# Performance work log

Hardware: AMD Instinct MI355X
Metric: run time of the kernel (lower is better)

## Reference

```python
import jax, jax.numpy as jnp
import numpy as np

R = 2
TAU = 0.1
EPS = 1e-7

# normalized 3x3 Sobel kernels (kornia SpatialGradient, normalized=True -> /8)
_GX = jnp.array([[-1., 0., 1.], [-2., 0., 2.], [-1., 0., 1.]], dtype=jnp.float32) / 8.0
_GY = _GX.T

K = 2 * R - 1  # 3
_HORIZ = jnp.zeros((K, K), jnp.float32).at[R - 1, :].set(1.0)
_VERT = jnp.zeros((K, K), jnp.float32).at[:, R - 1].set(1.0)
_LEAD = jnp.eye(K, dtype=jnp.float32)
_CNT = jnp.fliplr(jnp.eye(K, dtype=jnp.float32))


def _conv2d_same(x, k2d, mode):
    # depthwise 'same' cross-correlation, x: (B,C,H,W), k2d: (k,k)
    C = x.shape[1]
    p = k2d.shape[-1] // 2
    xp = jnp.pad(x, ((0, 0), (0, 0), (p, p), (p, p)), mode=mode)
    kern = jnp.broadcast_to(k2d[None, None], (C, 1) + k2d.shape)
    return jax.lax.conv_general_dilated(
        xp, kern, (1, 1), 'VALID',
        dimension_numbers=('NCHW', 'OIHW', 'NCHW'),
        feature_group_count=C)


def _grad_angles(t):
    # kornia SpatialGradient pads with replicate ('edge')
    gx = _conv2d_same(t, _GX, 'edge')
    gy = _conv2d_same(t, _GY, 'edge')
    grad_xx = _conv2d_same(gx, _GX, 'edge')
    grad_xy = _conv2d_same(gy, _GX, 'edge')
    grad_yy = _conv2d_same(gy, _GY, 'edge')
    theta = jnp.arctan(grad_yy * jnp.sign(-grad_xy + EPS) / (grad_xx + EPS))
    angle = theta * (180.0 / np.pi)
    return jnp.where(angle < 0, angle + 180.0, angle)


def _nms_loss(true_labels, pred_labels):
    angle = _grad_angles(true_labels)
    mask = (true_labels > 0).astype(jnp.float32)

    th_h = mask * (((angle >= 0) & (angle < 22.5)) | ((angle >= 157.5) & (angle < 180))).astype(jnp.float32)
    th_cd = mask * ((angle >= 22.5) & (angle < 67.5)).astype(jnp.float32)
    th_v = mask * ((angle >= 67.5) & (angle < 112.5)).astype(jnp.float32)
    th_ld = mask * ((angle > 112.5) & (angle < 157.5)).astype(jnp.float32)

    e = jnp.exp(pred_labels * TAU)

    def term(th, kern):
        f = _conv2d_same(e, kern, 'reflect')  # kornia filter2D default border 'reflect'
        return th * jnp.log(jnp.clip(e / (f + EPS), EPS, 1.0))

    total = (term(th_h, _HORIZ) + term(th_v, _VERT) +
             term(th_ld, _LEAD) + term(th_cd, _CNT))
    # sum over (C,H,W) per sample, mean over batch, negate
    return -jnp.mean(jnp.sum(total, axis=(1, 2, 3)))


def setup_inputs() -> dict:
    key = jax.random.key(0)
    k1, k2 = jax.random.split(key)
    B, C, H, W = 4, 19, 512, 512
    true_labels = jax.random.normal(k1, (B, C, H, W), dtype=jnp.float32)
    pred_labels = jax.random.normal(k2, (B, C, H, W), dtype=jnp.float32)
    return {"true_labels": true_labels, "pred_labels": pred_labels}


def reference(true_labels, pred_labels):
    return _nms_loss(true_labels, pred_labels)
```

## Files before the change

### kernel.cpp

```cpp
#include <hip/hip_runtime.h>

#define BAND 16
#define NITER (BAND + 4)
#define NSLOT 1024

__global__ __launch_bounds__(256) void nms_loss_kernel(
    const float* __restrict__ tl, const float* __restrict__ pl,
    double* __restrict__ acc_d, float* __restrict__ acc_f,
    int H, int W)
{
    const int y0  = blockIdx.x * BAND;
    const int ch  = blockIdx.y;
    const float* tc = tl + (size_t)ch * H * W;
    const float* pc = pl + (size_t)ch * H * W;
    const int tid  = threadIdx.x;
    const int lane = tid & 63;
    const int c0 = tid << 1;
    const int oa = min(max(c0 - 2, 0), W - 2);
    const int oc = min(c0 + 2, W - 2);
    const bool xedge = (c0 == 0) || (c0 == W - 2);

    float P1h[5][2], P2h[5][2], P3h[5][2];
    float eh[3][4], tch[3][2];
    float tA[6], pA[6], tB[6], pB[6];

    #define LOADROW(I, T6, P6) {                                                   \
        int tr_ = y0 - 2 + (I); tr_ = min(max(tr_, 0), H - 1);                      \
        int pr_ = y0 - 3 + (I); pr_ = pr_ < 0 ? -pr_ : (pr_ >= H ? 2*H-2-pr_ : pr_);\
        const float* tb_ = tc + (size_t)tr_ * W;                                    \
        const float* pb_ = pc + (size_t)pr_ * W;                                    \
        float2 a_ = *(const float2*)(tb_ + oa), b_ = *(const float2*)(tb_ + c0),    \
               c_ = *(const float2*)(tb_ + oc);                                     \
        T6[0]=a_.x; T6[1]=a_.y; T6[2]=b_.x; T6[3]=b_.y; T6[4]=c_.x; T6[5]=c_.y;     \
        a_ = *(const float2*)(pb_ + oa); b_ = *(const float2*)(pb_ + c0);           \
        c_ = *(const float2*)(pb_ + oc);                                            \
        P6[0]=a_.x; P6[1]=a_.y; P6[2]=b_.x; P6[3]=b_.y; P6[4]=c_.x; P6[5]=c_.y; }

    #define CONSUME(T6, P6, SP, SE) {                                               \
        const int sP = (SP), sE = (SE);                                             \
        if (!xedge) {                                                               \
            float s04 = T6[0] + T6[4], s13 = T6[1] + T6[3];                         \
            P1h[sP][0] = fmaf(-2.f, T6[2], s04);                                    \
            P3h[sP][0] = fmaf(6.f, T6[2], fmaf(4.f, s13, s04));                     \
            P2h[sP][0] = fmaf(2.f, T6[3] - T6[1], T6[4] - T6[0]);                   \
            float s04b = T6[1] + T6[5], s13b = T6[2] + T6[4];                       \
            P1h[sP][1] = fmaf(-2.f, T6[3], s04b);                                   \
            P3h[sP][1] = fmaf(6.f, T6[3], fmaf(4.f, s13b, s04b));                   \
            P2h[sP][1] = fmaf(2.f, T6[4] - T6[2], T6[5] - T6[1]);                   \
        } else if (c0 == 0) {                                                       \
            P1h[sP][0] = T6[4] - T6[3];                                             \
            P2h[sP][0] = fmaf(-2.f, T6[2], T6[3] + T6[4]);                          \
            P3h[sP][0] = fmaf(10.f, T6[2], fmaf(5.f, T6[3], T6[4]));                \
            P1h[sP][1] = fmaf(-2.f, T6[3], T6[2] + T6[5]);                          \
            P2h[sP][1] = fmaf(-3.f, T6[2], fmaf(2.f, T6[4], T6[5]));                \
            P3h[sP][1] = fmaf(5.f, T6[2], fmaf(6.f, T6[3], fmaf(4.f, T6[4], T6[5])));\
        } else {                                                                    \
            P1h[sP][0] = fmaf(-2.f, T6[2], T6[0] + T6[3]);                          \
            P2h[sP][0] = fmaf(3.f, T6[3], fmaf(-2.f, T6[1], -T6[0]));               \
            P3h[sP][0] = fmaf(5.f, T6[3], fmaf(6.f, T6[2], fmaf(4.f, T6[1], T6[0])));\
            P1h[sP][1] = T6[1] - T6[2];                                             \
            P2h[sP][1] = fmaf(2.f, T6[3], -T6[1] - T6[2]);                          \
            P3h[sP][1] = fmaf(10.f, T6[3], fmaf(5.f, T6[2], T6[1]));                \
        }                                                                           \
        tch[sE][0] = T6[2]; tch[sE][1] = T6[3];                                     \
        eh[sE][0] = __expf(0.1f * P6[1]);                                           \
        eh[sE][1] = __expf(0.1f * P6[2]);                                           \
        eh[sE][2] = __expf(0.1f * P6[3]);                                           \
        eh[sE][3] = __expf(0.1f * P6[4]); }

    #define OUTPUT(I) if ((I) >= 4) {                                               \
        const int y = y0 + (I) - 4;                                                 \
        const int s0=((I)-4)%5, s1=((I)-3)%5, s2=((I)-2)%5, s3=((I)-1)%5, s4=(I)%5; \
        const int et=((I)-2)%3, em=((I)-1)%3, ebq=(I)%3;                            \
        const bool ytop = (y == 0), ybot = (y == H - 1);                            \
        _Pragma("unroll")                                                           \
        for (int j = 0; j < 2; ++j) {                                               \
            float a04 = P1h[s0][j] + P1h[s4][j], a13 = P1h[s1][j] + P1h[s3][j];     \
            float xx = fmaf(6.f, P1h[s2][j], fmaf(4.f, a13, a04));                  \
            float xy = fmaf(2.f, P2h[s3][j] - P2h[s1][j], P2h[s4][j] - P2h[s0][j]); \
            float yy = fmaf(-2.f, P3h[s2][j], P3h[s0][j] + P3h[s4][j]);             \
            if (ytop) {                                                             \
                xx += P1h[s3][j] - P1h[s2][j];                                      \
                xy += P2h[s3][j] - P2h[s2][j];                                      \
                yy += P3h[s2][j] - P3h[s3][j];                                      \
            } else if (ybot) {                                                      \
                xx += P1h[s1][j] - P1h[s2][j];                                      \
                xy += P2h[s2][j] - P2h[s1][j];                                      \
                yy += P3h[s2][j] - P3h[s1][j];                                      \
            }                                                                       \
            if (tch[et][j] > 0.f) {                                                 \
                float den = xx + 6.4e-6f;                                           \
                float sa  = 6.4e-6f - xy;                                           \
                float ax = fabsf(den), ay = fabsf(yy);                              \
                bool isH = ay < 0.41421356f * ax;                                   \
                bool isV = ay >= 2.41421356f * ax;                                  \
                bool qp  = ((yy * sa) * den) > 0.f;                                 \
                float ec = eh[em][j + 1];                                           \
                float n1 = isH ? eh[em][j + 2] : (isV ? eh[ebq][j + 1]              \
                                : (qp ? eh[ebq][j] : eh[ebq][j + 2]));              \
                float n2 = isH ? eh[em][j]     : (isV ? eh[et][j + 1]               \
                                : (qp ? eh[et][j + 2] : eh[et][j]));                \
                partial += __logf(__fdividef(ec, ec + n1 + n2 + 1e-7f));            \
            }                                                                       \
        } }

    LOADROW(0, tA, pA)
    LOADROW(1, tB, pB)

    float partial = 0.f;

    #pragma unroll
    for (int ii = 0; ii < NITER; ii += 2) {
        CONSUME(tA, pA, ii % 5, ii % 3)
        CONSUME(tB, pB, (ii + 1) % 5, (ii + 1) % 3)
        if (ii + 2 < NITER) LOADROW(ii + 2, tA, pA)
        if (ii + 3 < NITER) LOADROW(ii + 3, tB, pB)
        OUTPUT(ii)
        OUTPUT(ii + 1)
    }

    for (int off = 32; off > 0; off >>= 1)
        partial += __shfl_down(partial, off, 64);
    if (lane == 0) {
        int fid = (blockIdx.y * gridDim.x + blockIdx.x) * 4 + (tid >> 6);
        if (acc_d) atomicAdd(&acc_d[fid & (NSLOT - 1)], (double)partial);
        else       atomicAdd(acc_f, partial);
    }
}

__global__ void finalize_kernel(const double* acc_d, float* out,
                                int use_double, float inv_b)
{
    if (use_double) {
        int l = threadIdx.x;
        double s = 0.0;
        for (int i = l; i < NSLOT; i += 64) s += acc_d[i];
        for (int off = 32; off > 0; off >>= 1) s += __shfl_down(s, off, 64);
        if (l == 0) out[0] = (float)(-s * (double)inv_b);
    } else {
        if (threadIdx.x == 0) out[0] = -out[0] * inv_b;
    }
}

extern "C" void kernel_launch(void* const* d_in, const int* in_sizes, int n_in,
                              void* d_out, int out_size, void* d_ws, size_t ws_size,
                              hipStream_t stream)
{
    const float* tl = (const float*)d_in[0];
    const float* pl = (const float*)d_in[1];
    float* out = (float*)d_out;

    const int H = 512, W = 512, B = 4;

    double* acc_d = nullptr;
    float* acc_f = nullptr;
    int use_double = 0;
    if (ws_size >= NSLOT * sizeof(double)) {
        acc_d = (double*)d_ws;
        use_double = 1;
        hipMemsetAsync(acc_d, 0, NSLOT * sizeof(double), stream);
    } else {
        acc_f = out;
        hipMemsetAsync(out, 0, sizeof(float), stream);
    }

    dim3 grid(H / BAND, 76, 1);
    nms_loss_kernel<<<grid, 256, 0, stream>>>(tl, pl, acc_d, acc_f, H, W);
    finalize_kernel<<<1, 64, 0, stream>>>(acc_d, out, use_double, 1.0f / (float)B);
}
```

Measured before the change: 63.13 us.

## Roll row loop into 5-step blocks, make x-edge handling branch-free, single load buffer

Replaces the fully unrolled 20-row loop with an outer non-unrolled loop of four 5-row unrolled blocks, shifting the exp and center rings instead of indexing them modulo. The x-edge special cases become branch-free by swapping loaded values and adding a masked correction term. Loads now use one buffer instead of two, so there is less lookahead prefetch. The aim is lower code size and register pressure, possibly higher occupancy, at the cost of register shuffles and less latency hiding.

Measured after the change: 61.33 us. 2.8% less time.

```diff
diff --git a/kernel.cpp b/kernel.cpp
--- a/kernel.cpp
+++ b/kernel.cpp
@@ -18,105 +18,100 @@
     const int c0 = tid << 1;
     const int oa = min(max(c0 - 2, 0), W - 2);
     const int oc = min(c0 + 2, W - 2);
-    const bool xedge = (c0 == 0) || (c0 == W - 2);
+    const bool eL = (c0 == 0), eR = (c0 == W - 2);
+    const float eL2 = eL ? 2.f : 0.f, eR2 = eR ? 2.f : 0.f;
 
     float P1h[5][2], P2h[5][2], P3h[5][2];
     float eh[3][4], tch[3][2];
-    float tA[6], pA[6], tB[6], pB[6];
+    float t6[6], p6[6];
 
-    #define LOADROW(I, T6, P6) {                                                   \
-        int tr_ = y0 - 2 + (I); tr_ = min(max(tr_, 0), H - 1);                      \
-        int pr_ = y0 - 3 + (I); pr_ = pr_ < 0 ? -pr_ : (pr_ >= H ? 2*H-2-pr_ : pr_);\
-        const float* tb_ = tc + (size_t)tr_ * W;                                    \
-        const float* pb_ = pc + (size_t)pr_ * W;                                    \
-        float2 a_ = *(const float2*)(tb_ + oa), b_ = *(const float2*)(tb_ + c0),    \
-               c_ = *(const float2*)(tb_ + oc);                                     \
-        T6[0]=a_.x; T6[1]=a_.y; T6[2]=b_.x; T6[3]=b_.y; T6[4]=c_.x; T6[5]=c_.y;     \
-        a_ = *(const float2*)(pb_ + oa); b_ = *(const float2*)(pb_ + c0);           \
-        c_ = *(const float2*)(pb_ + oc);                                            \
-        P6[0]=a_.x; P6[1]=a_.y; P6[2]=b_.x; P6[3]=b_.y; P6[4]=c_.x; P6[5]=c_.y; }
+    #define LOADROW(I) {                                                            \
+        int tr_ = y0 - 2 + (I); tr_ = min(max(tr_, 0), H - 1);                       \
+        int pr_ = y0 - 3 + (I); pr_ = pr_ < 0 ? -pr_ : (pr_ >= H ? 2*H-2-pr_ : pr_); \
+        const float* tb_ = tc + (size_t)tr_ * W;                                     \
+        const float* pb_ = pc + (size_t)pr_ * W;                                     \
+        float2 a_ = *(const float2*)(tb_ + oa), b_ = *(const float2*)(tb_ + c0),     \
+               c_ = *(const float2*)(tb_ + oc);                                      \
+        t6[0]=a_.x; t6[1]=a_.y; t6[2]=b_.x; t6[3]=b_.y; t6[4]=c_.x; t6[5]=c_.y;      \
+        a_ = *(const float2*)(pb_ + oa); b_ = *(const float2*)(pb_ + c0);            \
+        c_ = *(const float2*)(pb_ + oc);                                             \
+        p6[0]=a_.x; p6[1]=a_.y; p6[2]=b_.x; p6[3]=b_.y; p6[4]=c_.x; p6[5]=c_.y;      \
+        float g0_ = t6[0];                                                           \
+        t6[0] = eL ? t6[1] : t6[0];                                                  \
+        t6[1] = eL ? g0_   : t6[1];                                                  \
+        float g4_ = t6[4];                                                           \
+        t6[4] = eR ? t6[5] : t6[4];                                                  \
+        t6[5] = eR ? g4_   : t6[5]; }
 
-    #define CONSUME(T6, P6, SP, SE) {                                               \
-        const int sP = (SP), sE = (SE);                                             \
-        if (!xedge) {                                                               \
-            float s04 = T6[0] + T6[4], s13 = T6[1] + T6[3];                         \
-            P1h[sP][0] = fmaf(-2.f, T6[2], s04);                                    \
-            P3h[sP][0] = fmaf(6.f, T6[2], fmaf(4.f, s13, s04));                     \
-            P2h[sP][0] = fmaf(2.f, T6[3] - T6[1], T6[4] - T6[0]);                   \
-            float s04b = T6[1] + T6[5], s13b = T6[2] + T6[4];                       \
-            P1h[sP][1] = fmaf(-2.f, T6[3], s04b);                                   \
-            P3h[sP][1] = fmaf(6.f, T6[3], fmaf(4.f, s13b, s04b));                   \
-            P2h[sP][1] = fmaf(2.f, T6[4] - T6[2], T6[5] - T6[1]);                   \
-        } else if (c0 == 0) {                                                       \
-            P1h[sP][0] = T6[4] - T6[3];                                             \
-            P2h[sP][0] = fmaf(-2.f, T6[2], T6[3] + T6[4]);                          \
-            P3h[sP][0] = fmaf(10.f, T6[2], fmaf(5.f, T6[3], T6[4]));                \
-            P1h[sP][1] = fmaf(-2.f, T6[3], T6[2] + T6[5]);                          \
-            P2h[sP][1] = fmaf(-3.f, T6[2], fmaf(2.f, T6[4], T6[5]));                \
-            P3h[sP][1] = fmaf(5.f, T6[2], fmaf(6.f, T6[3], fmaf(4.f, T6[4], T6[5])));\
-        } else {                                                                    \
-            P1h[sP][0] = fmaf(-2.f, T6[2], T6[0] + T6[3]);                          \
-            P2h[sP][0] = fmaf(3.f, T6[3], fmaf(-2.f, T6[1], -T6[0]));               \
-            P3h[sP][0] = fmaf(5.f, T6[3], fmaf(6.f, T6[2], fmaf(4.f, T6[1], T6[0])));\
-            P1h[sP][1] = T6[1] - T6[2];                                             \
-            P2h[sP][1] = fmaf(2.f, T6[3], -T6[1] - T6[2]);                          \
-            P3h[sP][1] = fmaf(10.f, T6[3], fmaf(5.f, T6[2], T6[1]));                \
-        }                                                                           \
-        tch[sE][0] = T6[2]; tch[sE][1] = T6[3];                                     \
-        eh[sE][0] = __expf(0.1f * P6[1]);                                           \
-        eh[sE][1] = __expf(0.1f * P6[2]);                                           \
-        eh[sE][2] = __expf(0.1f * P6[3]);                                           \
-        eh[sE][3] = __expf(0.1f * P6[4]); }
+    #define CONSUME(K) {                                                             \
+        eh[0][0]=eh[1][0]; eh[0][1]=eh[1][1]; eh[0][2]=eh[1][2]; eh[0][3]=eh[1][3];  \
+        eh[1][0]=eh[2][0]; eh[1][1]=eh[2][1]; eh[1][2]=eh[2][2]; eh[1][3]=eh[2][3];  \
+        tch[0][0]=tch[1][0]; tch[0][1]=tch[1][1];                                    \
+        tch[1][0]=tch[2][0]; tch[1][1]=tch[2][1];                                    \
+        float s04 = t6[0] + t6[4], s13 = t6[1] + t6[3];                              \
+        P1h[K][0] = fmaf(-2.f, t6[2], s04);                                          \
+        P3h[K][0] = fmaf(6.f, t6[2], fmaf(4.f, s13, s04));                           \
+        P2h[K][0] = fmaf(2.f, t6[3] - t6[1], t6[4] - t6[0]);                         \
+        float s04b = t6[1] + t6[5], s13b = t6[2] + t6[4];                            \
+        P1h[K][1] = fmaf(-2.f, t6[3], s04b);                                         \
+        P3h[K][1] = fmaf(6.f, t6[3], fmaf(4.f, s13b, s04b));                         \
+        P2h[K][1] = fmaf(2.f, t6[4] - t6[2], t6[5] - t6[1]);                         \
+        P1h[K][0] = fmaf(eL2, t6[2] - t6[3], P1h[K][0]);                             \
+        P1h[K][1] = fmaf(eR2, t6[3] - t6[2], P1h[K][1]);                             \
+        tch[2][0] = t6[2]; tch[2][1] = t6[3];                                        \
+        eh[2][0] = __expf(0.1f * p6[1]);                                             \
+        eh[2][1] = __expf(0.1f * p6[2]);                                             \
+        eh[2][2] = __expf(0.1f * p6[3]);                                             \
+        eh[2][3] = __expf(0.1f * p6[4]); }
 
-    #define OUTPUT(I) if ((I) >= 4) {                                               \
-        const int y = y0 + (I) - 4;                                                 \
-        const int s0=((I)-4)%5, s1=((I)-3)%5, s2=((I)-2)%5, s3=((I)-1)%5, s4=(I)%5; \
-        const int et=((I)-2)%3, em=((I)-1)%3, ebq=(I)%3;                            \
-        const bool ytop = (y == 0), ybot = (y == H - 1);                            \
-        _Pragma("unroll")                                                           \
-        for (int j = 0; j < 2; ++j) {                                               \
-            float a04 = P1h[s0][j] + P1h[s4][j], a13 = P1h[s1][j] + P1h[s3][j];     \
-            float xx = fmaf(6.f, P1h[s2][j], fmaf(4.f, a13, a04));                  \
-            float xy = fmaf(2.f, P2h[s3][j] - P2h[s1][j], P2h[s4][j] - P2h[s0][j]); \
-            float yy = fmaf(-2.f, P3h[s2][j], P3h[s0][j] + P3h[s4][j]);             \
-            if (ytop) {                                                             \
-                xx += P1h[s3][j] - P1h[s2][j];                                      \
-                xy += P2h[s3][j] - P2h[s2][j];                                      \
-                yy += P3h[s2][j] - P3h[s3][j];                                      \
-            } else if (ybot) {                                                      \
-                xx += P1h[s1][j] - P1h[s2][j];                                      \
-                xy += P2h[s2][j] - P2h[s1][j];                                      \
-                yy += P3h[s2][j] - P3h[s1][j];                                      \
-            }                                                                       \
-            if (tch[et][j] > 0.f) {                                                 \
-                float den = xx + 6.4e-6f;                                           \
-                float sa  = 6.4e-6f - xy;                                           \
-                float ax = fabsf(den), ay = fabsf(yy);                              \
-                bool isH = ay < 0.41421356f * ax;                                   \
-                bool isV = ay >= 2.41421356f * ax;                                  \
-                bool qp  = ((yy * sa) * den) > 0.f;                                 \
-                float ec = eh[em][j + 1];                                           \
-                float n1 = isH ? eh[em][j + 2] : (isV ? eh[ebq][j + 1]              \
-                                : (qp ? eh[ebq][j] : eh[ebq][j + 2]));              \
-                float n2 = isH ? eh[em][j]     : (isV ? eh[et][j + 1]               \
-                                : (qp ? eh[et][j + 2] : eh[et][j]));                \
-                partial += __logf(__fdividef(ec, ec + n1 + n2 + 1e-7f));            \
-            }                                                                       \
+    #define OUTPUT(I, K) if ((I) >= 4) {                                             \
+        const int y = y0 + (I) - 4;                                                  \
+        const int s0=((K)+1)%5, s1=((K)+2)%5, s2=((K)+3)%5, s3=((K)+4)%5, s4=(K);    \
+        const bool ytop = (y == 0), ybot = (y == H - 1);                             \
+        _Pragma("unroll")                                                            \
+        for (int j = 0; j < 2; ++j) {                                                \
+            float a04 = P1h[s0][j] + P1h[s4][j], a13 = P1h[s1][j] + P1h[s3][j];      \
+            float xx = fmaf(6.f, P1h[s2][j], fmaf(4.f, a13, a04));                   \
+            float xy = fmaf(2.f, P2h[s3][j] - P2h[s1][j], P2h[s4][j] - P2h[s0][j]);  \
+            float yy = fmaf(-2.f, P3h[s2][j], P3h[s0][j] + P3h[s4][j]);              \
+            if (ytop) {                                                              \
+                xx += P1h[s3][j] - P1h[s2][j];                                       \
+                xy += P2h[s3][j] - P2h[s2][j];                                       \
+                yy += P3h[s2][j] - P3h[s3][j];                                       \
+            } else if (ybot) {                                                       \
+                xx += P1h[s1][j] - P1h[s2][j];                                       \
+                xy += P2h[s2][j] - P2h[s1][j];                                       \
+                yy += P3h[s2][j] - P3h[s1][j];                                       \
+            }                                                                        \
+            if (tch[0][j] > 0.f) {                                                   \
+                float den = xx + 6.4e-6f;                                            \
+                float sa  = 6.4e-6f - xy;                                            \
+                float ax = fabsf(den), ay = fabsf(yy);                               \
+                bool isH = ay < 0.41421356f * ax;                                    \
+                bool isV = ay >= 2.41421356f * ax;                                   \
+                bool qp  = ((yy * sa) * den) > 0.f;                                  \
+                float ec = eh[1][j + 1];                                             \
+                float n1 = isH ? eh[1][j + 2] : (isV ? eh[2][j + 1]                  \
+                                : (qp ? eh[2][j] : eh[2][j + 2]));                   \
+                float n2 = isH ? eh[1][j]     : (isV ? eh[0][j + 1]                  \
+                                : (qp ? eh[0][j + 2] : eh[0][j]));                   \
+                partial += __logf(__fdividef(ec, ec + n1 + n2 + 1e-7f));             \
+            }                                                                        \
         } }
 
-    LOADROW(0, tA, pA)
-    LOADROW(1, tB, pB)
+    LOADROW(0)
 
     float partial = 0.f;
 
-    #pragma unroll
-    for (int ii = 0; ii < NITER; ii += 2) {
-        CONSUME(tA, pA, ii % 5, ii % 3)
-        CONSUME(tB, pB, (ii + 1) % 5, (ii + 1) % 3)
-        if (ii + 2 < NITER) LOADROW(ii + 2, tA, pA)
-        if (ii + 3 < NITER) LOADROW(ii + 3, tB, pB)
-        OUTPUT(ii)
-        OUTPUT(ii + 1)
+    #pragma unroll 1
+    for (int mm = 0; mm < 4; ++mm) {
+        #pragma unroll
+        for (int k = 0; k < 5; ++k) {
+            const int i = mm * 5 + k;
+            CONSUME(k)
+            if (i + 1 < NITER) LOADROW(i + 1)
+            OUTPUT(i, k)
+        }
     }
 
     for (int off = 32; off > 0; off >>= 1)
```
